# Kernel tuning notes

Measured on AMD Instinct MI355X. Metric: run time of the kernel, lower is better.

## Reference

```python
import jax, jax.numpy as jnp
import numpy as np

N_ITEMS = 30000
N_HOPS = 2
TMP = 0.2
EPS = 1e-12


def _l2norm(x):
    # F.normalize(x, dim=1): x / max(||x||_2, eps)
    n = jnp.sqrt(jnp.sum(x * x, axis=1, keepdims=True))
    return x / jnp.maximum(n, EPS)


def setup_inputs() -> dict:
    key = jax.random.key(0)
    ks = jax.random.split(key, 12)
    n_users, n_entities, n_items, d = 50000, 100000, N_ITEMS, 64
    n_rel, n_fac, n_cls = 16, 4, 8
    n_edges, n_inter = 1000000, 500000
    return {
        'user_emb': jax.random.normal(ks[0], (n_users, d), jnp.float32),
        'entity_emb': jax.random.normal(ks[1], (n_entities, d), jnp.float32),
        'cls_emb': jax.random.normal(ks[2], (n_cls, d), jnp.float32),
        'latent_emb': jax.random.normal(ks[3], (n_fac, d), jnp.float32),
        'relation_emb': jax.random.normal(ks[4], (n_rel, d), jnp.float32),
        'disen_weight_att': jax.random.normal(ks[5], (n_fac, n_rel), jnp.float32),
        'edge_index': jax.random.randint(ks[6], (2, n_edges), 0, n_entities, jnp.int32),
        'edge_type': jax.random.randint(ks[7], (n_edges,), 0, n_rel, jnp.int32),
        'inter_user': jax.random.randint(ks[8], (n_inter,), 0, n_users, jnp.int32),
        'inter_item': jax.random.randint(ks[9], (n_inter,), 0, n_items, jnp.int32),
        'inter_val': jax.random.uniform(ks[10], (n_inter,), jnp.float32),
        'inter_cls': jax.random.randint(ks[11], (n_inter,), 0, n_cls, jnp.int32),
    }


def _cls_aggregate(entity_emb, user_emb, cls_emb, latent_emb, relation_emb,
                   disen_weight_att, edge_index, edge_type,
                   inter_user, inter_item, inter_val, inter_cls,
                   n_users, n_cls):
    n_entities = entity_emb.shape[0]
    item_emb = entity_emb[:N_ITEMS]
    # --- KG aggregate: scatter_mean over head of entity_emb[tail]*rel[edge_type]
    head, tail = edge_index[0], edge_index[1]
    msg = entity_emb[tail] * relation_emb[edge_type]            # [E, d]
    ent_sum = jax.ops.segment_sum(msg, head, num_segments=n_entities)
    cnt = jax.ops.segment_sum(jnp.ones_like(head, jnp.float32), head,
                              num_segments=n_entities)
    entity_agg = ent_sum / jnp.maximum(cnt, 1.0)[:, None]
    # --- user aggregate: sparse interact_mat @ item_emb
    u_msg = inter_val[:, None] * item_emb[inter_item]           # [I, d]
    user_agg = jax.ops.segment_sum(u_msg, inter_user, num_segments=n_users)
    # --- intent attention
    user_disen_att = jax.nn.softmax(user_emb @ latent_emb.T, axis=1)  # [U, F]
    disen_weight = jax.nn.softmax(disen_weight_att, axis=-1) @ relation_emb  # [F, d]
    user_agg = user_disen_att @ disen_weight + user_agg
    # --- class attention: inter_cls_mat[c] @ item_emb for each class
    user_cls_att = jax.nn.softmax(user_emb @ cls_emb.T, axis=1)  # [U, C]
    seg = inter_cls * n_users + inter_user
    user_cls = jax.ops.segment_sum(u_msg, seg, num_segments=n_cls * n_users)
    user_cls = user_cls.reshape(n_cls, n_users, -1)              # [C, U, d]
    user_agg = jnp.einsum('cud,uc->ud', user_cls, user_cls_att) + user_agg
    return entity_agg, user_agg


def _mutual_information(t, temperature):
    nt = _l2norm(t)
    scores = jnp.exp(nt @ nt.T / temperature)
    return -jnp.sum(jnp.log(jnp.diag(scores) / jnp.sum(scores, axis=1)))


def reference(user_emb, entity_emb, cls_emb, latent_emb, relation_emb,
              disen_weight_att, edge_index, edge_type, inter_user,
              inter_item, inter_val, inter_cls):
    n_users = user_emb.shape[0]
    n_cls = cls_emb.shape[0]
    entity_res, user_res = entity_emb, user_emb
    e, u = entity_emb, user_emb
    for _ in range(N_HOPS):
        e, u = _cls_aggregate(e, u, cls_emb, latent_emb, relation_emb,
                              disen_weight_att, edge_index, edge_type,
                              inter_user, inter_item, inter_val, inter_cls,
                              n_users, n_cls)
        e = _l2norm(e)
        u = _l2norm(u)
        entity_res = entity_res + e
        user_res = user_res + u
    cor_loss = _mutual_information(disen_weight_att, TMP)
    return entity_res, user_res, cor_loss
```

## Files before the change

kernel.cpp:

```cpp
#include <hip/hip_runtime.h>
#include <math.h>

typedef unsigned int uint;

constexpr int N_USERS  = 50000;
constexpr int N_ENT    = 100000;
constexpr int D        = 64;
constexpr int N_FAC    = 4;
constexpr int N_CLS    = 8;
constexpr int N_REL    = 16;
constexpr int N_EDGES  = 1000000;
constexpr int N_INTER  = 500000;

constexpr int BSH      = 7;
constexpr int SPB      = 1 << BSH;
constexpr int NBKT_E   = (N_ENT   + SPB - 1) / SPB;
constexpr int NBKT_U   = (N_USERS + SPB - 1) / SPB;
constexpr int CHUNK    = 4096;
constexpr int NB_E     = (N_EDGES + CHUNK - 1) / CHUNK;
constexpr int NB_U     = (N_INTER + CHUNK - 1) / CHUNK;
constexpr int EBUF_CAP = 3072;

typedef _Float16 h2_t __attribute__((ext_vector_type(2)));
union U32H2 { uint u; h2_t h; };

__device__ inline float h_lo(uint v) { U32H2 x; x.u = v; return (float)x.h.x; }
__device__ inline float h_hi(uint v) { U32H2 x; x.u = v; return (float)x.h.y; }
__device__ inline uint packh(float a, float b) {
    auto r = __builtin_amdgcn_cvt_pkrtz(a, b);
    union { decltype(r) h; uint u; } x;
    x.h = r;
    return x.u;
}

__device__ inline int wscan64_incl(int x, int lane) {
#pragma unroll
    for (int off = 1; off < 64; off <<= 1) {
        int v = __shfl_up(x, off, 64);
        if (lane >= off) x += v;
    }
    return x;
}

__device__ inline int block_scan_incl(int x, int* wsum) {
    int lane = threadIdx.x & 63, wv = threadIdx.x >> 6;
#pragma unroll
    for (int off = 1; off < 64; off <<= 1) {
        int v = __shfl_up(x, off, 64);
        if (lane >= off) x += v;
    }
    if (lane == 63) wsum[wv] = x;
    __syncthreads();
    if (wv == 0 && lane < 16) {
        int s = wsum[lane];
#pragma unroll
        for (int off = 1; off < 16; off <<= 1) {
            int v = __shfl_up(s, off, 64);
            if (lane >= off) s += v;
        }
        wsum[lane] = s;
    }
    __syncthreads();
    if (wv > 0) x += wsum[wv - 1];
    return x;
}

__global__ void k_convert(const float2* __restrict__ in, uint* __restrict__ out,
                          int n_src, int n_out) {
    for (int i = blockIdx.x * blockDim.x + threadIdx.x; i < n_out;
         i += gridDim.x * blockDim.x) {
        if (i < n_src) {
            float2 v = in[i];
            out[i] = packh(v.x, v.y);
        } else {
            out[i] = 0u;
        }
    }
}

__global__ void k_sort(const int* __restrict__ headE, const int* __restrict__ tailE,
                       const int* __restrict__ etype,
                       const int* __restrict__ iu, const int* __restrict__ ii,
                       const int* __restrict__ icls, const float* __restrict__ ival,
                       uint2* __restrict__ stagE, int* __restrict__ GE, int* __restrict__ RE,
                       uint2* __restrict__ stagU, int* __restrict__ GU, int* __restrict__ RU) {
    __shared__ int hist[NBKT_E];
    __shared__ int soff[NBKT_E + 1];
    __shared__ int cursor[NBKT_E];
    __shared__ int wsum[16];
    __shared__ uint2 sorted[CHUNK];
    int bid = blockIdx.x;
    bool isE = bid < NB_E;
    int blk  = isE ? bid : bid - NB_E;
    int n    = isE ? N_EDGES : N_INTER;
    int nbkt = isE ? NBKT_E : NBKT_U;
    int base = blk * CHUNK;
    int end  = min(base + CHUNK, n);
    int cblk = end - base;

    for (int b = threadIdx.x; b < nbkt; b += 256) hist[b] = 0;
    __syncthreads();

    uint2 ent[16]; int ebk[16];
#pragma unroll
    for (int j = 0; j < 16; ++j) {
        int i = base + threadIdx.x + j * 256;
        ebk[j] = -1;
        if (i < end) {
            uint x, y; int b;
            if (isE) {
                int h = headE[i];
                x = (uint)h; y = (uint)((tailE[i] << 4) | etype[i]); b = h >> BSH;
            } else {
                int u = iu[i];
                x = (uint)((u << 15) | ii[i]);
                y = (__float_as_uint(ival[i]) & ~7u) | (uint)icls[i];
                b = u >> BSH;
            }
            ent[j] = make_uint2(x, y); ebk[j] = b;
            atomicAdd(&hist[b], 1);
        }
    }
    __syncthreads();

    int b0 = threadIdx.x * 4;
    int lsum[4]; int mysum = 0;
#pragma unroll
    for (int j = 0; j < 4; ++j) {
        int b = b0 + j;
        int v = (b < nbkt) ? hist[b] : 0;
        lsum[j] = mysum; mysum += v;
    }
    int excl = block_scan_incl(mysum, wsum) - mysum;
#pragma unroll
    for (int j = 0; j < 4; ++j) {
        int b = b0 + j;
        if (b < nbkt) soff[b] = excl + lsum[j];
    }
    if (threadIdx.x == 0) soff[nbkt] = cblk;
    __syncthreads();
    for (int b = threadIdx.x; b < nbkt; b += 256) cursor[b] = soff[b];
    __syncthreads();

#pragma unroll
    for (int j = 0; j < 16; ++j) {
        if (ebk[j] >= 0) {
            int p = atomicAdd(&cursor[ebk[j]], 1);
            sorted[p] = ent[j];
        }
    }
    __syncthreads();

    uint2* stag = isE ? stagE : stagU;
    int* G = isE ? GE : GU;
    int* R = isE ? RE : RU;
    for (int i = threadIdx.x; i < cblk; i += 256) stag[blk * CHUNK + i] = sorted[i];
    for (int b = threadIdx.x; b < nbkt; b += 256) G[blk * nbkt + b] = hist[b];
    for (int b = threadIdx.x; b <= nbkt; b += 256) R[blk * (nbkt + 1) + b] = soff[b];
}

__global__ void k_bscanA(int* __restrict__ GE, int* __restrict__ totE,
                         int* __restrict__ GU, int* __restrict__ totU) {
    int bid = blockIdx.x;
    bool isE = bid < NBKT_E;
    int bkt  = isE ? bid : bid - NBKT_E;
    int NB   = isE ? NB_E : NB_U;
    int nbkt = isE ? NBKT_E : NBKT_U;
    int* G   = isE ? GE : GU;
    int* tot = isE ? totE : totU;
    int l = threadIdx.x;
    int carry = 0;
    for (int base = 0; base < NB; base += 64) {
        int x = (base + l < NB) ? G[(base + l) * nbkt + bkt] : 0;
        int incl = wscan64_incl(x, l);
        if (base + l < NB) G[(base + l) * nbkt + bkt] = carry + incl - x;
        carry += __shfl(incl, 63, 64);
    }
    if (l == 0) tot[bkt] = carry;
}

__device__ inline void scan_tot(const int* __restrict__ tot, int* __restrict__ base,
                                int nbkt, int l, int* __restrict__ off_last, int nseg) {
    int carry = 0;
    for (int b = 0; b < nbkt; b += 64) {
        int x = (b + l < nbkt) ? tot[b + l] : 0;
        int incl = wscan64_incl(x, l);
        if (b + l < nbkt) base[b + l] = carry + incl - x;
        carry += __shfl(incl, 63, 64);
    }
    if (l == 0) {
        base[nbkt] = carry;
        off_last[nseg] = carry;
        off_last[nseg + 1] = carry;
    }
}

__global__ void k_bscanB(const int* __restrict__ totE, int* __restrict__ baseE,
                         const int* __restrict__ totU, int* __restrict__ baseU,
                         int* __restrict__ eoff, int* __restrict__ uoff) {
    int t = threadIdx.x;
    if (t < 64) scan_tot(totE, baseE, NBKT_E, t, eoff, N_ENT);
    else        scan_tot(totU, baseU, NBKT_U, t - 64, uoff, N_USERS);
}

__global__ void k_final(const uint2* __restrict__ stagE, const int* __restrict__ GE,
                        const int* __restrict__ RE, const int* __restrict__ baseE,
                        const uint2* __restrict__ stagU, const int* __restrict__ GU,
                        const int* __restrict__ RU, const int* __restrict__ baseU,
                        int* __restrict__ eoff, int* __restrict__ uoff,
                        int* __restrict__ epay, int2* __restrict__ ipv) {
    __shared__ uint2 ebuf[EBUF_CAP];
    __shared__ int cnt[SPB], soff[SPB], cur[SPB];
    int bid = blockIdx.x;
    bool isE = bid < NBKT_E;
    int bkt = isE ? bid : bid - NBKT_E;
    const uint2* stag = isE ? stagE : stagU;
    const int* G  = isE ? GE : GU;
    const int* R  = isE ? RE : RU;
    const int* bb = isE ? baseE : baseU;
    int* off      = isE ? eoff : uoff;
    int NB   = isE ? NB_E : NB_U;
    int nbkt = isE ? NBKT_E : NBKT_U;
    int nseg = isE ? N_ENT : N_USERS;
    int r0 = bb[bkt], r1 = bb[bkt + 1];
    int bsz = r1 - r0;
    int t = threadIdx.x;
    if (t < SPB) cnt[t] = 0;
    for (int blk = t; blk < NB; blk += 256) {
        int rs  = R[blk * (nbkt + 1) + bkt];
        int re  = R[blk * (nbkt + 1) + bkt + 1];
        int dst = G[blk * nbkt + bkt];
        for (int j = rs; j < re; ++j) {
            int d = dst + (j - rs);
            if (d < EBUF_CAP) ebuf[d] = stag[blk * CHUNK + j];
        }
    }
    __syncthreads();
    for (int i = t; i < bsz; i += 256) {
        uint2 e = ebuf[i];
        int s = (int)(isE ? e.x : (e.x >> 15)) & (SPB - 1);
        atomicAdd(&cnt[s], 1);
    }
    __syncthreads();
    if (t < 64) {
        int a0 = cnt[2 * t], a1 = cnt[2 * t + 1];
        int incl = wscan64_incl(a0 + a1, t);
        int excl = incl - (a0 + a1);
        soff[2 * t] = excl;
        soff[2 * t + 1] = excl + a0;
    }
    __syncthreads();
    if (t < SPB) {
        cur[t] = soff[t];
        int seg = bkt * SPB + t;
        if (seg < nseg) off[seg] = r0 + soff[t];
    }
    __syncthreads();
    for (int i = t; i < bsz; i += 256) {
        uint2 e = ebuf[i];
        int s = (int)(isE ? e.x : (e.x >> 15)) & (SPB - 1);
        int pos = r0 + atomicAdd(&cur[s], 1);
        if (isE) {
            epay[pos] = (int)e.y;
        } else {
            int item = (int)(e.x & 0x7FFF), cls = (int)(e.y & 7u);
            ipv[pos] = make_int2((item << 3) | cls, (int)(e.y & ~7u));
        }
    }
}

__global__ void k_dw_loss(const float* __restrict__ datt,
                          const float* __restrict__ rel,
                          float* __restrict__ dw,
                          float* __restrict__ loss_out) {
    __shared__ float p[N_FAC][N_REL];
    __shared__ float nrm[N_FAC];
    __shared__ float sc[N_FAC][N_FAC];
    int t = threadIdx.x;
    if (t < N_FAC) {
        float m = -1e30f;
        for (int r = 0; r < N_REL; ++r) m = fmaxf(m, datt[t * N_REL + r]);
        float tmp[N_REL]; float s = 0.f;
        for (int r = 0; r < N_REL; ++r) { tmp[r] = expf(datt[t * N_REL + r] - m); s += tmp[r]; }
        for (int r = 0; r < N_REL; ++r) p[t][r] = tmp[r] / s;
        float ss = 0.f;
        for (int r = 0; r < N_REL; ++r) { float v = datt[t * N_REL + r]; ss += v * v; }
        nrm[t] = fmaxf(sqrtf(ss), 1e-12f);
    }
    __syncthreads();
    if (t < D) {
        for (int f = 0; f < N_FAC; ++f) {
            float acc = 0.f;
            for (int r = 0; r < N_REL; ++r) acc += p[f][r] * rel[r * D + t];
            dw[f * D + t] = acc;
        }
    }
    if (t < N_FAC * N_FAC) {
        int i = t >> 2, j = t & 3;
        float s = 0.f;
        for (int r = 0; r < N_REL; ++r) s += datt[i * N_REL + r] * datt[j * N_REL + r];
        s /= nrm[i] * nrm[j];
        sc[i][j] = expf(s * 5.0f);
    }
    __syncthreads();
    if (t == 0) {
        float loss = 0.f;
        for (int i = 0; i < N_FAC; ++i) {
            float rowsum = 0.f;
            for (int j = 0; j < N_FAC; ++j) rowsum += sc[i][j];
            loss += logf(sc[i][i] / rowsum);
        }
        *loss_out = -loss;
    }
}

template<bool F16>
__global__ void k_user_att(const void* __restrict__ uin,
                           const float* __restrict__ latent,
                           const float* __restrict__ cls,
                           float* __restrict__ att4,
                           float* __restrict__ att8) {
    int gid = blockIdx.x * blockDim.x + threadIdx.x;
    int row = gid >> 4;
    int lane = gid & 15;
    if (row >= N_USERS) return;
    float4 uv;
    if (F16) {
        uint2 q = ((const uint2*)uin)[row * 16 + lane];
        uv.x = h_lo(q.x); uv.y = h_hi(q.x); uv.z = h_lo(q.y); uv.w = h_hi(q.y);
    } else {
        uv = ((const float4*)uin)[row * 16 + lane];
    }
    float dots[12];
#pragma unroll
    for (int f = 0; f < 4; ++f) {
        float4 lv = ((const float4*)latent)[f * 16 + lane];
        dots[f] = uv.x*lv.x + uv.y*lv.y + uv.z*lv.z + uv.w*lv.w;
    }
#pragma unroll
    for (int c = 0; c < 8; ++c) {
        float4 cv = ((const float4*)cls)[c * 16 + lane];
        dots[4+c] = uv.x*cv.x + uv.y*cv.y + uv.z*cv.z + uv.w*cv.w;
    }
#pragma unroll
    for (int j = 0; j < 12; ++j) {
        float v = dots[j];
        for (int m = 1; m < 16; m <<= 1) v += __shfl_xor(v, m, 16);
        dots[j] = v;
    }
    float m4 = fmaxf(fmaxf(dots[0], dots[1]), fmaxf(dots[2], dots[3]));
    float e4v[4]; float s4 = 0.f;
#pragma unroll
    for (int f = 0; f < 4; ++f) { e4v[f] = expf(dots[f] - m4); s4 += e4v[f]; }
    float m8 = dots[4];
#pragma unroll
    for (int c = 1; c < 8; ++c) m8 = fmaxf(m8, dots[4+c]);
    float e8v[8]; float s8 = 0.f;
#pragma unroll
    for (int c = 0; c < 8; ++c) { e8v[c] = expf(dots[4+c] - m8); s8 += e8v[c]; }
    if (lane < 4) {
        float v = e4v[0];
#pragma unroll
        for (int f = 1; f < 4; ++f) if (lane == f) v = e4v[f];
        att4[row * 4 + lane] = v / s4;
    }
    if (lane < 8) {
        float v = e8v[0];
#pragma unroll
        for (int c = 1; c < 8; ++c) if (lane == c) v = e8v[c];
        att8[row * 8 + lane] = v / s8;
    }
}

__global__ __launch_bounds__(256)
void k_hop(const uint4* __restrict__ etab,
           const float4* __restrict__ entbase,
           const float4* __restrict__ usrbase,
           const float4* __restrict__ rel4,
           const int* __restrict__ eoff,
           const int* __restrict__ epay,
           const int* __restrict__ uoff,
           const int2* __restrict__ ipv,
           const float* __restrict__ att4,
           const float* __restrict__ att8,
           const float4* __restrict__ dw4,
           uint4* __restrict__ stateE,
           uint4* __restrict__ stateU,
           float4* __restrict__ outE,
           float4* __restrict__ outU,
           int mode) {
    int gid = blockIdx.x * 256 + threadIdx.x;
    int gw = gid >> 3;
    int k = threadIdx.x & 7;
    if (gw >= N_ENT + 1 + N_USERS) return;
    bool isEnt = gw <= N_ENT;
    float a0 = 0.f, a1 = 0.f, a2 = 0.f, a3 = 0.f;
    float a4 = 0.f, a5 = 0.f, a6 = 0.f, a7 = 0.f;

    if (isEnt) {
        int w = gw;
        int beg = eoff[w], end = eoff[w + 1];
        int nE = end - beg;
        const int* pp = epay + beg;
        for (int bse = 0; bse < nE; bse += 4) {
            int c = nE - bse;
            uint4 ev[4]; float4 ra[4], rb[4];
#pragma unroll
            for (int q = 0; q < 4; ++q) {
                int p = pp[bse + q];
                p = (q < c) ? p : (N_ENT << 4);
                ev[q] = etab[(((size_t)(p >> 4)) << 3) + k];
                const float4* rr = rel4 + ((p & 15) << 4) + (k << 1);
                ra[q] = rr[0]; rb[q] = rr[1];
            }
#pragma unroll
            for (int q = 0; q < 4; ++q) {
                a0 = fmaf(h_lo(ev[q].x), ra[q].x, a0);
                a1 = fmaf(h_hi(ev[q].x), ra[q].y, a1);
                a2 = fmaf(h_lo(ev[q].y), ra[q].z, a2);
                a3 = fmaf(h_hi(ev[q].y), ra[q].w, a3);
                a4 = fmaf(h_lo(ev[q].z), rb[q].x, a4);
                a5 = fmaf(h_hi(ev[q].z), rb[q].y, a5);
                a6 = fmaf(h_lo(ev[q].w), rb[q].z, a6);
                a7 = fmaf(h_hi(ev[q].w), rb[q].w, a7);
            }
        }
        float ss = a0*a0 + a1*a1 + a2*a2 + a3*a3 + a4*a4 + a5*a5 + a6*a6 + a7*a7;
#pragma unroll
        for (int m = 1; m < 8; m <<= 1) ss += __shfl_xor(ss, m, 8);
        float s = 1.0f / fmaxf(sqrtf(ss), 1e-12f);
        float v0 = a0*s, v1 = a1*s, v2 = a2*s, v3 = a3*s;
        float v4 = a4*s, v5 = a5*s, v6 = a6*s, v7 = a7*s;
        if (mode == 0) {
            stateE[((size_t)w << 3) + k] =
                make_uint4(packh(v0, v1), packh(v2, v3), packh(v4, v5), packh(v6, v7));
        } else if (w < N_ENT) {
            size_t b = ((size_t)w << 4) + (k << 1);
            float4 b0 = entbase[b], b1 = entbase[b + 1];
            uint4 own = etab[((size_t)w << 3) + k];
            float4 o0 = make_float4(b0.x + h_lo(own.x) + v0, b0.y + h_hi(own.x) + v1,
                                    b0.z + h_lo(own.y) + v2, b0.w + h_hi(own.y) + v3);
            float4 o1 = make_float4(b1.x + h_lo(own.z) + v4, b1.y + h_hi(own.z) + v5,
                                    b1.z + h_lo(own.w) + v6, b1.w + h_hi(own.w) + v7);
            outE[b] = o0; outE[b + 1] = o1;
        }
    } else {
        int w = gw - (N_ENT + 1);
        int beg = uoff[w], end = uoff[w + 1];
        int nE = end - beg;
        const int2* pv = ipv + beg;
        float a8v = att8[w * 8 + k];
        for (int bse = 0; bse < nE; bse += 4) {
            int c = nE - bse;
            uint4 ev[4]; float wg[4];
#pragma unroll
            for (int q = 0; q < 4; ++q) {
                int2 e = pv[bse + q];
                int p = e.x;
                int pe = (q < c) ? p : 0;
                ev[q] = etab[(((size_t)(pe >> 3)) << 3) + k];
                float wgt = __int_as_float(e.y) * (1.0f + __shfl(a8v, p & 7, 8));
                wg[q] = (q < c) ? wgt : 0.0f;
            }
#pragma unroll
            for (int q = 0; q < 4; ++q) {
                a0 = fmaf(h_lo(ev[q].x), wg[q], a0);
                a1 = fmaf(h_hi(ev[q].x), wg[q], a1);
                a2 = fmaf(h_lo(ev[q].y), wg[q], a2);
                a3 = fmaf(h_hi(ev[q].y), wg[q], a3);
                a4 = fmaf(h_lo(ev[q].z), wg[q], a4);
                a5 = fmaf(h_hi(ev[q].z), wg[q], a5);
                a6 = fmaf(h_lo(ev[q].w), wg[q], a6);
                a7 = fmaf(h_hi(ev[q].w), wg[q], a7);
            }
        }
#pragma unroll
        for (int f = 0; f < 4; ++f) {
            float a = att4[w * 4 + f];
            const float4* dd = dw4 + f * 16 + (k << 1);
            float4 d0 = dd[0], d1 = dd[1];
            a0 = fmaf(a, d0.x, a0); a1 = fmaf(a, d0.y, a1);
            a2 = fmaf(a, d0.z, a2); a3 = fmaf(a, d0.w, a3);
            a4 = fmaf(a, d1.x, a4); a5 = fmaf(a, d1.y, a5);
            a6 = fmaf(a, d1.z, a6); a7 = fmaf(a, d1.w, a7);
        }
        float ss = a0*a0 + a1*a1 + a2*a2 + a3*a3 + a4*a4 + a5*a5 + a6*a6 + a7*a7;
#pragma unroll
        for (int m = 1; m < 8; m <<= 1) ss += __shfl_xor(ss, m, 8);
        float s = 1.0f / fmaxf(sqrtf(ss), 1e-12f);
        float v0 = a0*s, v1 = a1*s, v2 = a2*s, v3 = a3*s;
        float v4 = a4*s, v5 = a5*s, v6 = a6*s, v7 = a7*s;
        if (mode == 0) {
            stateU[((size_t)w << 3) + k] =
                make_uint4(packh(v0, v1), packh(v2, v3), packh(v4, v5), packh(v6, v7));
        } else {
            size_t b = ((size_t)w << 4) + (k << 1);
            float4 b0 = usrbase[b], b1 = usrbase[b + 1];
            uint4 own = stateU[((size_t)w << 3) + k];
            float4 o0 = make_float4(b0.x + h_lo(own.x) + v0, b0.y + h_hi(own.x) + v1,
                                    b0.z + h_lo(own.y) + v2, b0.w + h_hi(own.y) + v3);
            float4 o1 = make_float4(b1.x + h_lo(own.z) + v4, b1.y + h_hi(own.z) + v5,
                                    b1.z + h_lo(own.w) + v6, b1.w + h_hi(own.w) + v7);
            outU[b] = o0; outU[b + 1] = o1;
        }
    }
}

extern "C" void kernel_launch(void* const* d_in, const int* in_sizes, int n_in,
                              void* d_out, int out_size, void* d_ws, size_t ws_size,
                              hipStream_t stream) {
    const float* user_emb   = (const float*)d_in[0];
    const float* entity_emb = (const float*)d_in[1];
    const float* cls_emb    = (const float*)d_in[2];
    const float* latent_emb = (const float*)d_in[3];
    const float* rel_emb    = (const float*)d_in[4];
    const float* disen      = (const float*)d_in[5];
    const int*   edge_index = (const int*)d_in[6];
    const int*   edge_type  = (const int*)d_in[7];
    const int*   inter_user = (const int*)d_in[8];
    const int*   inter_item = (const int*)d_in[9];
    const float* inter_val  = (const float*)d_in[10];
    const int*   inter_cls  = (const int*)d_in[11];

    float* out      = (float*)d_out;
    float* out_ent  = out;
    float* out_user = out + (size_t)N_ENT * D;
    float* out_loss = out + (size_t)N_ENT * D + (size_t)N_USERS * D;

    char* w = (char*)d_ws;
    auto alloc = [&](size_t bytes) -> char* {
        char* p = w;
        w += (bytes + 255) & ~(size_t)255;
        return p;
    };
    uint*  ebuf0 = (uint*)alloc((size_t)(N_ENT + 1) * 32 * 4);
    uint*  eA    = (uint*)alloc((size_t)(N_ENT + 1) * 32 * 4);
    uint*  uA    = (uint*)alloc((size_t)N_USERS * 32 * 4);
    int*   epay  = (int*)alloc((size_t)(N_EDGES + 16) * 4);
    int2*  ipv   = (int2*)alloc((size_t)(N_INTER + 16) * 8);
    int*   eoff  = (int*)alloc((size_t)(N_ENT + 4) * 4);
    int*   uoff  = (int*)alloc((size_t)(N_USERS + 4) * 4);
    int*   GE    = (int*)alloc((size_t)NB_E * NBKT_E * 4);
    int*   RE    = (int*)alloc((size_t)NB_E * (NBKT_E + 1) * 4);
    int*   GU    = (int*)alloc((size_t)NB_U * NBKT_U * 4);
    int*   RU    = (int*)alloc((size_t)NB_U * (NBKT_U + 1) * 4);
    int*   totE  = (int*)alloc((size_t)NBKT_E * 4);
    int*   totU  = (int*)alloc((size_t)NBKT_U * 4);
    int*   baseE = (int*)alloc((size_t)(NBKT_E + 1) * 4);
    int*   baseU = (int*)alloc((size_t)(NBKT_U + 1) * 4);
    float* att4  = (float*)alloc((size_t)N_USERS * N_FAC * 4);
    float* att8  = (float*)alloc((size_t)N_USERS * N_CLS * 4);
    float* dw    = (float*)alloc((size_t)N_FAC * D * 4);

    uint2* stagE = (uint2*)eA;
    uint2* stagU = (uint2*)uA;

    const int* head = edge_index;
    const int* tail = edge_index + N_EDGES;

    k_convert<<<2048, 256, 0, stream>>>((const float2*)entity_emb, ebuf0,
                                        N_ENT * 32, (N_ENT + 1) * 32);
    k_dw_loss<<<1, 64, 0, stream>>>(disen, rel_emb, dw, out_loss);

    k_sort  <<<NB_E + NB_U, 256, 0, stream>>>(head, tail, edge_type,
                                              inter_user, inter_item, inter_cls, inter_val,
                                              stagE, GE, RE, stagU, GU, RU);
    k_bscanA<<<NBKT_E + NBKT_U, 64, 0, stream>>>(GE, totE, GU, totU);
    k_bscanB<<<1, 128, 0, stream>>>(totE, baseE, totU, baseU, eoff, uoff);
    k_final <<<NBKT_E + NBKT_U, 256, 0, stream>>>(stagE, GE, RE, baseE,
                                                  stagU, GU, RU, baseU,
                                                  eoff, uoff, epay, ipv);

    const int att_blocks = (N_USERS * 16 + 255) / 256;
    const int hop_blocks = ((N_ENT + 1 + N_USERS) * 8 + 255) / 256;

    k_user_att<false><<<att_blocks, 256, 0, stream>>>(user_emb, latent_emb, cls_emb, att4, att8);
    k_hop<<<hop_blocks, 256, 0, stream>>>((const uint4*)ebuf0, nullptr, nullptr,
                                          (const float4*)rel_emb, eoff, epay, uoff, ipv,
                                          att4, att8, (const float4*)dw,
                                          (uint4*)eA, (uint4*)uA, nullptr, nullptr, 0);

    k_user_att<true><<<att_blocks, 256, 0, stream>>>(uA, latent_emb, cls_emb, att4, att8);
    k_hop<<<hop_blocks, 256, 0, stream>>>((const uint4*)eA,
                                          (const float4*)entity_emb, (const float4*)user_emb,
                                          (const float4*)rel_emb, eoff, epay, uoff, ipv,
                                          att4, att8, (const float4*)dw,
                                          nullptr, (uint4*)uA,
                                          (float4*)out_ent, (float4*)out_user, 1);
}
```

Measured before the change: 155.9 us.

## Sort rows by degree within 256-row tiles and prefetch next edge indices

A new kernel buckets each 256-row tile of entities and users by degree, largest first, and writes a packed descriptor (start offset, degree, row id). The hop kernel reads these descriptors, so rows of similar length share a wavefront and fewer lanes sit idle at the tail of each gather loop. The edge-index loads for the next group of four are also software-prefetched. This adds a small launch and extra descriptor traffic, and the prefetch reads past each row's end, which relies on the padded buffers.

```diff
diff --git a/kernel.cpp b/kernel.cpp
--- a/kernel.cpp
+++ b/kernel.cpp
@@ -20,6 +20,10 @@
 constexpr int NB_E     = (N_EDGES + CHUNK - 1) / CHUNK;
 constexpr int NB_U     = (N_INTER + CHUNK - 1) / CHUNK;
 constexpr int EBUF_CAP = 3072;
+
+constexpr int E_ROWS   = N_ENT + 1;
+constexpr int NW_E     = (E_ROWS  + 255) / 256;
+constexpr int NW_U     = (N_USERS + 255) / 256;
 
 typedef _Float16 h2_t __attribute__((ext_vector_type(2)));
 union U32H2 { uint u; h2_t h; };
@@ -213,7 +217,7 @@
     __shared__ int cnt[SPB], soff[SPB], cur[SPB];
     int bid = blockIdx.x;
     bool isE = bid < NBKT_E;
-    int bkt = isE ? bid : bid - NBKT_E;
+    int bkt = bid < NBKT_E ? bid : bid - NBKT_E;
     const uint2* stag = isE ? stagE : stagU;
     const int* G  = isE ? GE : GU;
     const int* R  = isE ? RE : RU;
@@ -269,6 +273,40 @@
     }
 }
 
+__global__ void k_rowsort(const int* __restrict__ eoff, const int* __restrict__ uoff,
+                          uint2* __restrict__ rdE, uint2* __restrict__ rdU) {
+    __shared__ int hist[64], cur[64];
+    int bid = blockIdx.x;
+    bool isE = bid < NW_E;
+    const int* off = isE ? eoff : uoff;
+    uint2* rd = isE ? rdE : rdU;
+    int nseg = isE ? E_ROWS : N_USERS;
+    int w0 = (isE ? bid : bid - NW_E) * 256;
+    int t = threadIdx.x;
+    if (t < 64) hist[t] = 0;
+    __syncthreads();
+    int s = w0 + t;
+    int b = -1, beg = 0, d = 0;
+    if (s < nseg) {
+        beg = off[s];
+        d = off[s + 1] - beg;
+        b = min(d, 63);
+        atomicAdd(&hist[b], 1);
+    }
+    __syncthreads();
+    if (t < 64) {
+        int rb = 63 - t;
+        int x = hist[rb];
+        int incl = wscan64_incl(x, t);
+        cur[rb] = incl - x;
+    }
+    __syncthreads();
+    if (b >= 0) {
+        int pos = atomicAdd(&cur[b], 1);
+        rd[w0 + pos] = make_uint2((uint)beg, ((uint)d << 18) | (uint)s);
+    }
+}
+
 __global__ void k_dw_loss(const float* __restrict__ datt,
                           const float* __restrict__ rel,
                           float* __restrict__ dw,
@@ -377,9 +415,9 @@
            const float4* __restrict__ entbase,
            const float4* __restrict__ usrbase,
            const float4* __restrict__ rel4,
-           const int* __restrict__ eoff,
+           const uint2* __restrict__ rdE,
            const int* __restrict__ epay,
-           const int* __restrict__ uoff,
+           const uint2* __restrict__ rdU,
            const int2* __restrict__ ipv,
            const float* __restrict__ att4,
            const float* __restrict__ att8,
@@ -392,23 +430,29 @@
     int gid = blockIdx.x * 256 + threadIdx.x;
     int gw = gid >> 3;
     int k = threadIdx.x & 7;
-    if (gw >= N_ENT + 1 + N_USERS) return;
-    bool isEnt = gw <= N_ENT;
+    if (gw >= E_ROWS + N_USERS) return;
+    bool isEnt = gw < E_ROWS;
     float a0 = 0.f, a1 = 0.f, a2 = 0.f, a3 = 0.f;
     float a4 = 0.f, a5 = 0.f, a6 = 0.f, a7 = 0.f;
 
     if (isEnt) {
-        int w = gw;
-        int beg = eoff[w], end = eoff[w + 1];
-        int nE = end - beg;
+        uint2 rdv = rdE[gw];
+        int beg = (int)rdv.x;
+        int nE  = (int)(rdv.y >> 18);
+        int w   = (int)(rdv.y & 0x3FFFFu);
         const int* pp = epay + beg;
+        int pc[4];
+#pragma unroll
+        for (int q = 0; q < 4; ++q) pc[q] = pp[q];
         for (int bse = 0; bse < nE; bse += 4) {
             int c = nE - bse;
+            int pn[4];
+#pragma unroll
+            for (int q = 0; q < 4; ++q) pn[q] = pp[bse + 4 + q];
             uint4 ev[4]; float4 ra[4], rb[4];
 #pragma unroll
             for (int q = 0; q < 4; ++q) {
-                int p = pp[bse + q];
-                p = (q < c) ? p : (N_ENT << 4);
+                int p = (q < c) ? pc[q] : (N_ENT << 4);
                 ev[q] = etab[(((size_t)(p >> 4)) << 3) + k];
                 const float4* rr = rel4 + ((p & 15) << 4) + (k << 1);
                 ra[q] = rr[0]; rb[q] = rr[1];
@@ -424,6 +468,8 @@
                 a6 = fmaf(h_lo(ev[q].w), rb[q].z, a6);
                 a7 = fmaf(h_hi(ev[q].w), rb[q].w, a7);
             }
+#pragma unroll
+            for (int q = 0; q < 4; ++q) pc[q] = pn[q];
         }
         float ss = a0*a0 + a1*a1 + a2*a2 + a3*a3 + a4*a4 + a5*a5 + a6*a6 + a7*a7;
 #pragma unroll
@@ -445,21 +491,27 @@
             outE[b] = o0; outE[b + 1] = o1;
         }
     } else {
-        int w = gw - (N_ENT + 1);
-        int beg = uoff[w], end = uoff[w + 1];
-        int nE = end - beg;
+        uint2 rdv = rdU[gw - E_ROWS];
+        int beg = (int)rdv.x;
+        int nE  = (int)(rdv.y >> 18);
+        int w   = (int)(rdv.y & 0x3FFFFu);
         const int2* pv = ipv + beg;
         float a8v = att8[w * 8 + k];
+        int2 ec[4];
+#pragma unroll
+        for (int q = 0; q < 4; ++q) ec[q] = pv[q];
         for (int bse = 0; bse < nE; bse += 4) {
             int c = nE - bse;
+            int2 en[4];
+#pragma unroll
+            for (int q = 0; q < 4; ++q) en[q] = pv[bse + 4 + q];
             uint4 ev[4]; float wg[4];
 #pragma unroll
             for (int q = 0; q < 4; ++q) {
-                int2 e = pv[bse + q];
-                int p = e.x;
+                int p = ec[q].x;
                 int pe = (q < c) ? p : 0;
                 ev[q] = etab[(((size_t)(pe >> 3)) << 3) + k];
-                float wgt = __int_as_float(e.y) * (1.0f + __shfl(a8v, p & 7, 8));
+                float wgt = __int_as_float(ec[q].y) * (1.0f + __shfl(a8v, p & 7, 8));
                 wg[q] = (q < c) ? wgt : 0.0f;
             }
 #pragma unroll
@@ -473,6 +525,8 @@
                 a6 = fmaf(h_lo(ev[q].w), wg[q], a6);
                 a7 = fmaf(h_hi(ev[q].w), wg[q], a7);
             }
+#pragma unroll
+            for (int q = 0; q < 4; ++q) ec[q] = en[q];
         }
 #pragma unroll
         for (int f = 0; f < 4; ++f) {
@@ -533,13 +587,15 @@
         w += (bytes + 255) & ~(size_t)255;
         return p;
     };
-    uint*  ebuf0 = (uint*)alloc((size_t)(N_ENT + 1) * 32 * 4);
-    uint*  eA    = (uint*)alloc((size_t)(N_ENT + 1) * 32 * 4);
+    uint*  ebuf0 = (uint*)alloc((size_t)E_ROWS * 32 * 4);
+    uint*  eA    = (uint*)alloc((size_t)E_ROWS * 32 * 4);
     uint*  uA    = (uint*)alloc((size_t)N_USERS * 32 * 4);
     int*   epay  = (int*)alloc((size_t)(N_EDGES + 16) * 4);
     int2*  ipv   = (int2*)alloc((size_t)(N_INTER + 16) * 8);
     int*   eoff  = (int*)alloc((size_t)(N_ENT + 4) * 4);
     int*   uoff  = (int*)alloc((size_t)(N_USERS + 4) * 4);
+    uint2* rdE   = (uint2*)alloc((size_t)NW_E * 256 * 8);
+    uint2* rdU   = (uint2*)alloc((size_t)NW_U * 256 * 8);
     int*   GE    = (int*)alloc((size_t)NB_E * NBKT_E * 4);
     int*   RE    = (int*)alloc((size_t)NB_E * (NBKT_E + 1) * 4);
     int*   GU    = (int*)alloc((size_t)NB_U * NBKT_U * 4);
@@ -559,7 +615,7 @@
     const int* tail = edge_index + N_EDGES;
 
     k_convert<<<2048, 256, 0, stream>>>((const float2*)entity_emb, ebuf0,
-                                        N_ENT * 32, (N_ENT + 1) * 32);
+                                        N_ENT * 32, E_ROWS * 32);
     k_dw_loss<<<1, 64, 0, stream>>>(disen, rel_emb, dw, out_loss);
 
     k_sort  <<<NB_E + NB_U, 256, 0, stream>>>(head, tail, edge_type,
@@ -570,20 +626,21 @@
     k_final <<<NBKT_E + NBKT_U, 256, 0, stream>>>(stagE, GE, RE, baseE,
                                                   stagU, GU, RU, baseU,
                                                   eoff, uoff, epay, ipv);
+    k_rowsort<<<NW_E + NW_U, 256, 0, stream>>>(eoff, uoff, rdE, rdU);
 
     const int att_blocks = (N_USERS * 16 + 255) / 256;
-    const int hop_blocks = ((N_ENT + 1 + N_USERS) * 8 + 255) / 256;
+    const int hop_blocks = ((E_ROWS + N_USERS) * 8 + 255) / 256;
 
     k_user_att<false><<<att_blocks, 256, 0, stream>>>(user_emb, latent_emb, cls_emb, att4, att8);
     k_hop<<<hop_blocks, 256, 0, stream>>>((const uint4*)ebuf0, nullptr, nullptr,
-                                          (const float4*)rel_emb, eoff, epay, uoff, ipv,
+                                          (const float4*)rel_emb, rdE, epay, rdU, ipv,
                                           att4, att8, (const float4*)dw,
                                           (uint4*)eA, (uint4*)uA, nullptr, nullptr, 0);
 
     k_user_att<true><<<att_blocks, 256, 0, stream>>>(uA, latent_emb, cls_emb, att4, att8);
     k_hop<<<hop_blocks, 256, 0, stream>>>((const uint4*)eA,
                                           (const float4*)entity_emb, (const float4*)user_emb,
-                                          (const float4*)rel_emb, eoff, epay, uoff, ipv,
+                                          (const float4*)rel_emb, rdE, epay, rdU, ipv,
                                           att4, att8, (const float4*)dw,
                                           nullptr, (uint4*)uA,
                                           (float4*)out_ent, (float4*)out_user, 1);
```

Result: slower. 167.5 us (+7.5%).
